# Kernel optimization log

Hardware: AMD Instinct MI355X
Metric: run time of the kernel (lower is better)

## Reference

```python
import jax, jax.numpy as jnp
import numpy as np

K = 3
KK = K * K


def conv3x3(x, w, b):
    # x: [B,C,H,W], w: [O,C,3,3]
    y = jax.lax.conv_general_dilated(x, w, (1, 1), ((1, 1), (1, 1)),
                                     dimension_numbers=('NCHW', 'OIHW', 'NCHW'))
    return y + b[None, :, None, None]


def deform_conv(x, offset, w, b):
    # torchvision.ops.deform_conv2d, 3x3, pad=1, stride=1, no mask.
    B, C, H, W = x.shape
    off = offset.reshape(B, KK, 2, H, W)  # per kernel tap: (dy, dx)
    ky = jnp.repeat(jnp.arange(K, dtype=x.dtype) - 1, K)  # [9]
    kx = jnp.tile(jnp.arange(K, dtype=x.dtype) - 1, K)
    py = jnp.arange(H, dtype=x.dtype)[None, None, :, None] + ky[None, :, None, None] + off[:, :, 0]
    px = jnp.arange(W, dtype=x.dtype)[None, None, None, :] + kx[None, :, None, None] + off[:, :, 1]
    y0 = jnp.floor(py)
    x0 = jnp.floor(px)
    wy = (py - y0)[:, None]  # [B,1,9,H,W]
    wx = (px - x0)[:, None]
    y0i = y0.astype(jnp.int32)
    x0i = x0.astype(jnp.int32)
    xf = x.reshape(B, C, H * W)

    def corner(yi, xi):
        valid = ((yi >= 0) & (yi < H) & (xi >= 0) & (xi < W))
        idx = jnp.clip(yi, 0, H - 1) * W + jnp.clip(xi, 0, W - 1)  # [B,9,H,W]
        g = jax.vmap(lambda xb, ib: xb[:, ib.reshape(-1)])(xf, idx)  # [B,C,9*H*W]
        return g.reshape(B, C, KK, H, W) * valid[:, None].astype(x.dtype)

    val = (corner(y0i, x0i) * (1 - wy) * (1 - wx)
           + corner(y0i, x0i + 1) * (1 - wy) * wx
           + corner(y0i + 1, x0i) * wy * (1 - wx)
           + corner(y0i + 1, x0i + 1) * wy * wx)  # [B,C,9,H,W]
    out = jnp.einsum('bckhw,ock->bohw', val, w.reshape(w.shape[0], C, KK))
    return out + b[None, :, None, None]


def se_gate(x, w1, b1, w2, b2):
    # global avg pool -> 1x1 conv -> relu -> 1x1 conv -> sigmoid -> scale
    m = x.mean((2, 3))  # [B,C]
    h = jax.nn.relu(jnp.einsum('bc,rc->br', m, w1) + b1)
    g = jax.nn.sigmoid(jnp.einsum('br,cr->bc', h, w2) + b2)
    return x * g[:, :, None, None]


def resize_bilinear(x, oh, ow):
    # F.interpolate(mode='bilinear', align_corners=False)
    B, C, H, W = x.shape

    def coords(n_in, n_out):
        src = (jnp.arange(n_out, dtype=x.dtype) + 0.5) * (n_in / n_out) - 0.5
        src = jnp.clip(src, 0.0, n_in - 1)
        i0 = jnp.floor(src).astype(jnp.int32)
        i1 = jnp.minimum(i0 + 1, n_in - 1)
        return i0, i1, (src - i0).astype(x.dtype)

    y0, y1, wy = coords(H, oh)
    x = x[:, :, y0, :] * (1 - wy)[None, None, :, None] + x[:, :, y1, :] * wy[None, None, :, None]
    c0, c1, wc = coords(W, ow)
    x = x[:, :, :, c0] * (1 - wc)[None, None, None, :] + x[:, :, :, c1] * wc[None, None, None, :]
    return x


def setup_inputs() -> dict:
    key = jax.random.key(0)
    ks = jax.random.split(key, 12)
    B, C, H, W = 4, 64, 128, 128
    L, O, R = 4, 64, 4  # levels, out_channels, reduction=64//16
    d = {
        'x': jax.random.normal(ks[0], (B, C, H, W), jnp.float32),
        'off_w': jax.random.normal(ks[1], (L, 2 * KK, C, 3, 3), jnp.float32) * 0.01,
        'off_b': jax.random.normal(ks[2], (L, 2 * KK), jnp.float32) * 0.01,
        'dc_w': jax.random.normal(ks[3], (L, O, C, 3, 3), jnp.float32) * 0.05,
        'dc_b': jax.random.normal(ks[4], (L, O), jnp.float32) * 0.05,
        'se_w1': jax.random.normal(ks[5], (L, R, O), jnp.float32) * 0.1,
        'se_b1': jax.random.normal(ks[6], (L, R), jnp.float32) * 0.1,
        'se_w2': jax.random.normal(ks[7], (L, O, R), jnp.float32) * 0.1,
        'se_b2': jax.random.normal(ks[8], (L, O), jnp.float32) * 0.1,
        'fuse_w': jax.random.normal(ks[9], (O, L * O), jnp.float32) * 0.05,
        'fuse_b': jax.random.normal(ks[10], (O,), jnp.float32) * 0.05,
    }
    return d


def reference(x, off_w, off_b, dc_w, dc_b, se_w1, se_b1, se_w2, se_b2, fuse_w, fuse_b):
    B, _, H, W = x.shape
    L = off_w.shape[0]
    cur = x
    feats = []
    for i in range(L):
        if i > 0:
            cur = resize_bilinear(cur, cur.shape[2] // 2, cur.shape[3] // 2)
        off = conv3x3(cur, off_w[i], off_b[i])
        cur = deform_conv(cur, off, dc_w[i], dc_b[i])
        cur = se_gate(cur, se_w1[i], se_b1[i], se_w2[i], se_b2[i])
        feats.append(resize_bilinear(cur, H, W))
    for i in range(L - 2, -1, -1):
        feats[i] = feats[i] + feats[i + 1]
    fused = jnp.concatenate(feats, axis=1)  # [B, L*O, H, W]
    return jnp.einsum('bchw,oc->bohw', fused, fuse_w) + fuse_b[None, :, None, None]
```

## Files before the change

### kernel.cpp

```cpp
#include <hip/hip_runtime.h>
#include <hip/hip_bf16.h>
#include <math.h>


constexpr int Bn = 4;

typedef __attribute__((ext_vector_type(8))) short short8;
typedef __attribute__((ext_vector_type(4))) float f32x4;
typedef __attribute__((ext_vector_type(4))) unsigned uint4v;

static __device__ __forceinline__ short f2b(float f){
  union { float f; unsigned u; } v; v.f = f;
  unsigned r = v.u + 0x7fffu + ((v.u >> 16) & 1u);
  return (short)(r >> 16);
}
static __device__ __forceinline__ unsigned f2b2(float x, float y){
  union { __hip_bfloat162 h; unsigned u; } cv;
  cv.h = __float22bfloat162_rn(make_float2(x, y));
  return cv.u;
}

constexpr size_t OFF_CUR   = 0;
constexpr size_t OFF_DC    = OFF_CUR  + 4194304;
constexpr size_t OFF_T0    = OFF_DC   + 4194304;
constexpr size_t OFF_T1    = OFF_T0   + 4194304;
constexpr size_t OFF_T2    = OFF_T1   + 1048576;
constexpr size_t OFF_T3    = OFF_T2   + 262144;
constexpr size_t OFF_WSUMT = OFF_T3   + 65536;
constexpr size_t OFF_DCWT  = OFF_WSUMT + 8192;
constexpr size_t OFF_OWT   = OFF_DCWT  + 73728;
constexpr size_t OFF_SUMS  = OFF_OWT   + 36864;

__global__ void prep_k(const float* __restrict__ dc_w, const float* __restrict__ off_w,
                       const float* __restrict__ fuse_w, float* __restrict__ ws){
  int i = blockIdx.x * 256 + threadIdx.x;
  short* dcwT  = (short*)(ws + OFF_DCWT);
  short* owT   = (short*)(ws + OFF_OWT);
  short* wsumT = (short*)(ws + OFF_WSUMT);
  if (i < 147456){
    int oc = i / 576, r = i % 576, k = r >> 6, c = r & 63;
    dcwT[i] = f2b(dc_w[(oc*64 + c)*9 + k]);
  } else if (i < 147456 + 73728){
    int t = i - 147456;
    int lm = t / 576, l = lm >> 5, m = lm & 31, r = t % 576, k = r >> 6, c = r & 63;
    owT[t] = (m < 18) ? f2b(off_w[((l*18 + m)*64 + c)*9 + k]) : (short)0;
  } else if (i < 147456 + 73728 + 16384){
    int t = i - (147456 + 73728);
    int l = t / 4096, r = t % 4096, o = r / 64, c = r % 64;
    float s = 0.f;
    for (int jl = 0; jl <= l; jl++) s += fuse_w[o*256 + jl*64 + c];
    wsumT[t] = f2b(s);
  } else if (i < 147456 + 73728 + 16384 + 65536){
    ws[OFF_SUMS + (i - (147456 + 73728 + 16384))] = 0.f;
  }
}

__global__ __launch_bounds__(256) void cvt_k(const float* __restrict__ x, float* __restrict__ cur){
  __shared__ float t[64][65];
  int tile = blockIdx.x;
  int b = tile >> 8, p0 = (tile & 255) << 6;
  int tx = threadIdx.x & 63, ty = threadIdx.x >> 6;
  #pragma unroll
  for (int c = ty; c < 64; c += 4)
    t[c][tx] = x[(((size_t)(b << 6) + c) << 14) + p0 + tx];
  __syncthreads();
  #pragma unroll
  for (int pp = ty; pp < 64; pp += 4)
    cur[(((size_t)(b << 14)) + p0 + pp) * 64 + tx] = t[tx][pp];
}

template<int H, int LVL>
__global__ __launch_bounds__(256, 6) void deform_k(
    const float* __restrict__ cur, const float* __restrict__ ws_all,
    const float* __restrict__ off_bias, const float* __restrict__ dc_bias,
    float* __restrict__ dc, float* __restrict__ sums){
  constexpr int W = H, P = H * W;
  constexpr int PITCHB = 584 * 2;
  __shared__ __align__(16) short valA[16][584];
  __shared__ float offsP[2][16][18];
  __shared__ float4 tapW[144];
  __shared__ int4   tapI[144];
  const short* owt = (const short*)(ws_all + OFF_OWT) + LVL * 32 * 576;
  const short* dcw = (const short*)(ws_all + OFF_DCWT) + (size_t)LVL * 64 * 576;
  const int tid = threadIdx.x;
  const int wave = tid >> 6, lane = tid & 63;
  const int c0 = lane & 15, quad = lane >> 4, q4 = quad * 4;
  const int half = lane >> 5, cc = lane & 31;
  const int pix0 = blockIdx.x * 16;
  const int b = pix0 / P, pb = pix0 % P;
  const int hrow = pb / W, wcol = pb % W;
  const float* curb = cur + (size_t)b * P * 64;
  const char* curc = (const char*)curb + cc * 8;
  char* valc = (char*)valA + wave * (4 * PITCHB);

  #pragma unroll
  for (int i = 0; i < 18; i++){
    const int t0 = 2*i, t1 = t0 + 1;
    const int p0 = t0/9, k0 = t0%9, p1 = t1/9, k1 = t1%9;
    int yy0 = hrow + k0/3 - 1, xx0 = wcol + wave*4 + p0 + k0%3 - 1;
    int yy1 = hrow + k1/3 - 1, xx1 = wcol + wave*4 + p1 + k1%3 - 1;
    bool v0 = ((unsigned)yy0 < (unsigned)H) & ((unsigned)xx0 < (unsigned)W);
    bool v1 = ((unsigned)yy1 < (unsigned)H) & ((unsigned)xx1 < (unsigned)W);
    int  i0 = v0 ? (yy0*W + xx0) : 0,  i1 = v1 ? (yy1*W + xx1) : 0;
    float m0 = v0 ? 1.f : 0.f,         m1 = v1 ? 1.f : 0.f;
    int   idx = half ? i1 : i0;
    float m   = half ? m1 : m0;
    float2 v = *(const float2*)(curc + (size_t)idx * 256);
    unsigned pk = f2b2(v.x * m, v.y * m);
    const int ob0 = p0*PITCHB + k0*128, ob1 = p1*PITCHB + k1*128;
    *(unsigned*)(valc + (half ? ob1 : ob0) + cc*4) = pk;
  }
  __syncthreads();

  {
    const int colw = wave & 1, kh = wave >> 1;
    f32x4 oacc = {0,0,0,0};
    #pragma unroll
    for (int kb = 0; kb < 9; kb++){
      int kk = kh*9 + kb;
      short8 a  = *(const short8*)&valA[c0][kk*32 + quad*8];
      short8 bf = *(const short8*)&owt[(colw*16 + c0)*576 + kk*32 + quad*8];
      oacc = __builtin_amdgcn_mfma_f32_16x16x32_bf16(a, bf, oacc, 0, 0, 0);
    }
    int comp = colw*16 + c0;
    if (comp < 18){
      #pragma unroll
      for (int r = 0; r < 4; r++) offsP[kh][q4 + r][comp] = oacc[r];
    }
  }
  __syncthreads();

  if (tid < 144){
    int p = tid / 9, k = tid % 9;
    int h = hrow, w = wcol + p;
    float oy = offsP[0][p][2*k]     + offsP[1][p][2*k]     + off_bias[LVL*18 + 2*k];
    float ox = offsP[0][p][2*k + 1] + offsP[1][p][2*k + 1] + off_bias[LVL*18 + 2*k + 1];
    float py = (float)(h + k/3 - 1) + oy;
    float px = (float)(w + k%3 - 1) + ox;
    float y0f = floorf(py), x0f = floorf(px);
    float fy = py - y0f, fx = px - x0f;
    int y0 = (int)y0f, x0 = (int)x0f, y1 = y0 + 1, x1 = x0 + 1;
    bool vy0 = (y0 >= 0) & (y0 < H), vy1 = (y1 >= 0) & (y1 < H);
    bool vx0 = (x0 >= 0) & (x0 < W), vx1 = (x1 >= 0) & (x1 < W);
    int y0c = min(max(y0, 0), H-1), y1c = min(max(y1, 0), H-1);
    int x0c = min(max(x0, 0), W-1), x1c = min(max(x1, 0), W-1);
    float gy = 1.f - fy, gx = 1.f - fx;
    tapW[tid] = make_float4((vy0 & vx0) ? gy*gx : 0.f,
                            (vy0 & vx1) ? gy*fx : 0.f,
                            (vy1 & vx0) ? fy*gx : 0.f,
                            (vy1 & vx1) ? fy*fx : 0.f);
    tapI[tid] = make_int4((y0c*W + x0c) << 8, (y0c*W + x1c) << 8,
                          (y1c*W + x0c) << 8, (y1c*W + x1c) << 8);
  }
  __syncthreads();

  #pragma unroll
  for (int i = 0; i < 18; i++){
    int T = wave*36 + 2*i + half;
    float4 wv = tapW[T];
    int4   ti = tapI[T];
    float2 a0 = *(const float2*)(curc + ti.x);
    float2 a1 = *(const float2*)(curc + ti.y);
    float2 a2 = *(const float2*)(curc + ti.z);
    float2 a3 = *(const float2*)(curc + ti.w);
    float vx = wv.x*a0.x + wv.y*a1.x + wv.z*a2.x + wv.w*a3.x;
    float vy = wv.x*a0.y + wv.y*a1.y + wv.z*a2.y + wv.w*a3.y;
    unsigned pk = f2b2(vx, vy);
    const int t0 = 2*i, t1 = t0 + 1;
    const int ob0 = (t0/9)*PITCHB + (t0%9)*128, ob1 = (t1/9)*PITCHB + (t1%9)*128;
    *(unsigned*)(valc + (half ? ob1 : ob0) + cc*4) = pk;
  }
  __syncthreads();

  const int n = wave*16 + c0;
  float bt = dc_bias[LVL*64 + n];
  f32x4 d0 = {bt, bt, bt, bt}, d1 = {0,0,0,0};
  #pragma unroll
  for (int kb = 0; kb < 9; kb++){
    short8 a  = *(const short8*)&valA[c0][kb*32 + quad*8];
    short8 bf = *(const short8*)&dcw[n*576 + kb*32 + quad*8];
    d0 = __builtin_amdgcn_mfma_f32_16x16x32_bf16(a, bf, d0, 0, 0, 0);
  }
  #pragma unroll
  for (int kb = 9; kb < 18; kb++){
    short8 a  = *(const short8*)&valA[c0][kb*32 + quad*8];
    short8 bf = *(const short8*)&dcw[n*576 + kb*32 + quad*8];
    d1 = __builtin_amdgcn_mfma_f32_16x16x32_bf16(a, bf, d1, 0, 0, 0);
  }
  f32x4 acc;
  #pragma unroll
  for (int r = 0; r < 4; r++) acc[r] = d0[r] + d1[r];
  float* dcb = dc + (size_t)pix0 * 64;
  #pragma unroll
  for (int r = 0; r < 4; r++) dcb[(q4 + r)*64 + n] = acc[r];
  float s = acc[0] + acc[1] + acc[2] + acc[3];
  s += __shfl_xor(s, 16);
  s += __shfl_xor(s, 32);
  if (quad == 0) atomicAdd(&sums[(LVL*16 + (blockIdx.x & 15))*256 + (b << 6) + n], s);
}

template<int W, int LVL>
__global__ __launch_bounds__(256) void fuse_gd_k(
    const float* __restrict__ dcv, const float* __restrict__ sums,
    const float* __restrict__ se_w1, const float* __restrict__ se_b1,
    const float* __restrict__ se_w2, const float* __restrict__ se_b2,
    const float* __restrict__ ws_all, float* __restrict__ tmp, float* __restrict__ curn){
  constexpr int P = W * W;
  constexpr bool POOL = (LVL < 3);
  constexpr float invP = 1.f / (float)P;
  __shared__ __align__(16) float fS[64][68];
  __shared__ __align__(16) float gsh[64];
  const short* wsl = (const short*)(ws_all + OFF_WSUMT) + LVL * 4096;
  const int tid = threadIdx.x, wave = tid >> 6, lane = tid & 63;
  const int c0 = lane & 15, quad = lane >> 4, q4 = quad * 4;
  int b, rp = 0, cs = 0;
  if (POOL){
    constexpr int tilesPerB = P / 64, tilesPerRow = W / 32;
    b = blockIdx.x / tilesPerB;
    int r = blockIdx.x % tilesPerB;
    rp = r / tilesPerRow; cs = r % tilesPerRow;
  } else {
    b = (blockIdx.x * 64) / P;
  }

  {
    int sg = tid >> 6, c = tid & 63;
    float part = 0.f;
    #pragma unroll
    for (int s = 0; s < 4; s++) part += sums[(LVL*16 + sg*4 + s)*256 + (b << 6) + c];
    fS[sg][c] = part;
    __syncthreads();
    if (tid < 64){
      int r = tid & 3, j = tid >> 2;
      float hp = 0.f;
      #pragma unroll
      for (int q = 0; q < 4; q++){
        int cq = j*4 + q;
        float m = (fS[0][cq] + fS[1][cq] + fS[2][cq] + fS[3][cq]) * invP;
        hp += m * se_w1[(LVL*4 + r)*64 + cq];
      }
      hp += __shfl_xor(hp, 4);  hp += __shfl_xor(hp, 8);
      hp += __shfl_xor(hp, 16); hp += __shfl_xor(hp, 32);
      float hr = fmaxf(hp + se_b1[LVL*4 + r], 0.f);
      float a = se_b2[LVL*64 + tid];
      #pragma unroll
      for (int r2 = 0; r2 < 4; r2++)
        a += __shfl(hr, r2) * se_w2[(LVL*64 + tid)*4 + r2];
      gsh[tid] = 1.f / (1.f + expf(-a));
    }
    __syncthreads();
  }

  float4 g4 = *(const float4*)&gsh[c0*4];
  #pragma unroll
  for (int i = 0; i < 4; i++){
    int lp = wave*16 + (lane >> 4) + i*4;
    size_t gpix = POOL ? ((size_t)b*P + (size_t)(2*rp + (lp >> 5))*W + cs*32 + (lp & 31))
                       : ((size_t)blockIdx.x*64 + lp);
    float4 d = *(const float4*)&dcv[gpix*64 + c0*4];
    float4 v = make_float4(d.x*g4.x, d.y*g4.y, d.z*g4.z, d.w*g4.w);
    *(float4*)&fS[lp][c0*4] = v;
  }
  __syncthreads();
  f32x4 acc[4] = {{0,0,0,0},{0,0,0,0},{0,0,0,0},{0,0,0,0}};
  #pragma unroll
  for (int kb = 0; kb < 2; kb++){
    float4 lo = *(const float4*)&fS[wave*16 + c0][kb*32 + quad*8];
    float4 hi = *(const float4*)&fS[wave*16 + c0][kb*32 + quad*8 + 4];
    uint4v ua = {f2b2(lo.x, lo.y), f2b2(lo.z, lo.w), f2b2(hi.x, hi.y), f2b2(hi.z, hi.w)};
    short8 a = __builtin_bit_cast(short8, ua);
    #pragma unroll
    for (int t = 0; t < 4; t++){
      short8 bf = *(const short8*)&wsl[(t*16 + c0)*64 + kb*32 + quad*8];
      acc[t] = __builtin_amdgcn_mfma_f32_16x16x32_bf16(a, bf, acc[t], 0, 0, 0);
    }
  }
  #pragma unroll
  for (int t = 0; t < 4; t++){
    int n = t*16 + c0;
    size_t plane = ((size_t)(b << 6) + n) * P;
    size_t pix = POOL ? ((size_t)(2*rp + (wave >> 1))*W + cs*32 + (wave & 1)*16 + q4)
                      : ((size_t)(blockIdx.x*64) - (size_t)b*P + wave*16 + q4);
    *(f32x4*)&tmp[plane + pix] = acc[t];
  }
  if constexpr (POOL){
    int j = tid >> 4, uu = tid & 15;
    float4 p0 = *(const float4*)&fS[2*j][uu*4];
    float4 p1 = *(const float4*)&fS[2*j + 1][uu*4];
    float4 p2 = *(const float4*)&fS[32 + 2*j][uu*4];
    float4 p3 = *(const float4*)&fS[33 + 2*j][uu*4];
    float4 av = make_float4(0.25f*(p0.x + p1.x + p2.x + p3.x),
                            0.25f*(p0.y + p1.y + p2.y + p3.y),
                            0.25f*(p0.z + p1.z + p2.z + p3.z),
                            0.25f*(p0.w + p1.w + p2.w + p3.w));
    *(float4*)&curn[((size_t)b*(P/4) + (size_t)rp*(W/2) + cs*16 + j)*64 + uu*4] = av;
  }
}

__global__ void final_k(const float* __restrict__ ws_all, const float* __restrict__ fuse_bias,
                        float* __restrict__ out){
  int i = blockIdx.x * 256 + threadIdx.x;
  int w = i & 127, h = (i >> 7) & 127, o = (i >> 14) & 63, b = i >> 20;
  float acc = fuse_bias[o] + ws_all[OFF_T0 + (((size_t)(b << 6) + o) << 14) + (h << 7) + w];
  const float* tarr[3] = {ws_all + OFF_T1, ws_all + OFF_T2, ws_all + OFF_T3};
  #pragma unroll
  for (int li = 0; li < 3; li++){
    int l = li + 1, Hl = 128 >> l;
    float scale = 1.0f / (float)(1 << l);
    float sy = fminf(fmaxf((h + 0.5f)*scale - 0.5f, 0.f), (float)(Hl - 1));
    float sx = fminf(fmaxf((w + 0.5f)*scale - 0.5f, 0.f), (float)(Hl - 1));
    int y0 = (int)sy, x0 = (int)sx;
    float fy = sy - y0, fx = sx - x0;
    int y1 = min(y0 + 1, Hl - 1), x1 = min(x0 + 1, Hl - 1);
    const float* tb = tarr[li] + (size_t)((b << 6) + o) * Hl * Hl;
    float v00 = tb[y0*Hl + x0], v01 = tb[y0*Hl + x1];
    float v10 = tb[y1*Hl + x0], v11 = tb[y1*Hl + x1];
    acc += (1.f-fy)*((1.f-fx)*v00 + fx*v01) + fy*((1.f-fx)*v10 + fx*v11);
  }
  out[i] = acc;
}

extern "C" void kernel_launch(void* const* d_in, const int* in_sizes, int n_in,
                              void* d_out, int out_size, void* d_ws, size_t ws_size,
                              hipStream_t stream){
  (void)in_sizes; (void)n_in; (void)out_size; (void)ws_size;
  const float* x      = (const float*)d_in[0];
  const float* off_w  = (const float*)d_in[1];
  const float* off_b  = (const float*)d_in[2];
  const float* dc_w   = (const float*)d_in[3];
  const float* dc_b   = (const float*)d_in[4];
  const float* se_w1  = (const float*)d_in[5];
  const float* se_b1  = (const float*)d_in[6];
  const float* se_w2  = (const float*)d_in[7];
  const float* se_b2  = (const float*)d_in[8];
  const float* fuse_w = (const float*)d_in[9];
  const float* fuse_b = (const float*)d_in[10];
  float* out = (float*)d_out;
  float* ws = (float*)d_ws;
  float* cur  = ws + OFF_CUR;
  float* dc   = ws + OFF_DC;
  float* tmp[4] = {ws + OFF_T0, ws + OFF_T1, ws + OFF_T2, ws + OFF_T3};
  float* sums = ws + OFF_SUMS;

  prep_k<<<(303104 + 255)/256, 256, 0, stream>>>(dc_w, off_w, fuse_w, ws);
  cvt_k<<<1024, 256, 0, stream>>>(x, cur);

  deform_k<128,0><<<4096, 256, 0, stream>>>(cur, ws, off_b, dc_b, dc, sums);
  fuse_gd_k<128,0><<<1024, 256, 0, stream>>>(dc, sums, se_w1, se_b1, se_w2, se_b2, ws, tmp[0], cur);
  deform_k<64,1><<<1024, 256, 0, stream>>>(cur, ws, off_b, dc_b, dc, sums);
  fuse_gd_k<64,1><<<256, 256, 0, stream>>>(dc, sums, se_w1, se_b1, se_w2, se_b2, ws, tmp[1], cur);
  deform_k<32,2><<<256, 256, 0, stream>>>(cur, ws, off_b, dc_b, dc, sums);
  fuse_gd_k<32,2><<<64, 256, 0, stream>>>(dc, sums, se_w1, se_b1, se_w2, se_b2, ws, tmp[2], cur);
  deform_k<16,3><<<64, 256, 0, stream>>>(cur, ws, off_b, dc_b, dc, sums);
  fuse_gd_k<16,3><<<16, 256, 0, stream>>>(dc, sums, se_w1, se_b1, se_w2, se_b2, ws, tmp[3], nullptr);

  final_k<<<16384, 256, 0, stream>>>(ws, fuse_b, out);
}
```

Before: 273.3 us.

## Store intermediate activations as bf16 and tile deform blocks as 4x4 pixel squares

The NHWC activation buffer feeding the deformable conv is now packed as bf16 pairs instead of fp32, in both the initial transpose and the pooled output of the fuse kernel. This halves gather bytes for the 3x3 taps and the bilinear corner samples. Each block also now covers a 4x4 spatial tile instead of 16 pixels in one row, which should improve cache locality of the neighbour gathers. The cost is an extra rounding of the input to bf16 before the bilinear interpolation, which slightly changes numerics.

```diff
diff --git a/kernel.cpp b/kernel.cpp
--- a/kernel.cpp
+++ b/kernel.cpp
@@ -19,6 +19,8 @@
   cv.h = __float22bfloat162_rn(make_float2(x, y));
   return cv.u;
 }
+static __device__ __forceinline__ float blo(unsigned u){ return __uint_as_float(u << 16); }
+static __device__ __forceinline__ float bhi(unsigned u){ return __uint_as_float(u & 0xffff0000u); }
 
 constexpr size_t OFF_CUR   = 0;
 constexpr size_t OFF_DC    = OFF_CUR  + 4194304;
@@ -55,7 +57,7 @@
   }
 }
 
-__global__ __launch_bounds__(256) void cvt_k(const float* __restrict__ x, float* __restrict__ cur){
+__global__ __launch_bounds__(256) void cvt_k(const float* __restrict__ x, unsigned* __restrict__ cur){
   __shared__ float t[64][65];
   int tile = blockIdx.x;
   int b = tile >> 8, p0 = (tile & 255) << 6;
@@ -64,18 +66,23 @@
   for (int c = ty; c < 64; c += 4)
     t[c][tx] = x[(((size_t)(b << 6) + c) << 14) + p0 + tx];
   __syncthreads();
-  #pragma unroll
-  for (int pp = ty; pp < 64; pp += 4)
-    cur[(((size_t)(b << 14)) + p0 + pp) * 64 + tx] = t[tx][pp];
+  int u = threadIdx.x & 31, pr = threadIdx.x >> 5;
+  #pragma unroll
+  for (int i = 0; i < 8; i++){
+    int pp = pr + i*8;
+    unsigned v = f2b2(t[2*u][pp], t[2*u + 1][pp]);
+    cur[((size_t)(b << 14) + p0 + pp)*32 + u] = v;
+  }
 }
 
 template<int H, int LVL>
 __global__ __launch_bounds__(256, 6) void deform_k(
-    const float* __restrict__ cur, const float* __restrict__ ws_all,
+    const unsigned* __restrict__ cur, const float* __restrict__ ws_all,
     const float* __restrict__ off_bias, const float* __restrict__ dc_bias,
     float* __restrict__ dc, float* __restrict__ sums){
   constexpr int W = H, P = H * W;
   constexpr int PITCHB = 584 * 2;
+  constexpr int TPR = W/4, TPB = P/16;
   __shared__ __align__(16) short valA[16][584];
   __shared__ float offsP[2][16][18];
   __shared__ float4 tapW[144];
@@ -86,29 +93,27 @@
   const int wave = tid >> 6, lane = tid & 63;
   const int c0 = lane & 15, quad = lane >> 4, q4 = quad * 4;
   const int half = lane >> 5, cc = lane & 31;
-  const int pix0 = blockIdx.x * 16;
-  const int b = pix0 / P, pb = pix0 % P;
-  const int hrow = pb / W, wcol = pb % W;
-  const float* curb = cur + (size_t)b * P * 64;
-  const char* curc = (const char*)curb + cc * 8;
+  const int b = blockIdx.x / TPB;
+  const int rr = blockIdx.x % TPB;
+  const int hrow = (rr / TPR) * 4, wcol = (rr % TPR) * 4;
+  const char* curc = (const char*)(cur + (size_t)b * P * 32) + cc * 4;
   char* valc = (char*)valA + wave * (4 * PITCHB);
 
   #pragma unroll
   for (int i = 0; i < 18; i++){
     const int t0 = 2*i, t1 = t0 + 1;
-    const int p0 = t0/9, k0 = t0%9, p1 = t1/9, k1 = t1%9;
-    int yy0 = hrow + k0/3 - 1, xx0 = wcol + wave*4 + p0 + k0%3 - 1;
-    int yy1 = hrow + k1/3 - 1, xx1 = wcol + wave*4 + p1 + k1%3 - 1;
+    const int p0l = t0/9, k0 = t0%9, p1l = t1/9, k1 = t1%9;
+    int yy0 = hrow + wave + k0/3 - 1, xx0 = wcol + p0l + k0%3 - 1;
+    int yy1 = hrow + wave + k1/3 - 1, xx1 = wcol + p1l + k1%3 - 1;
     bool v0 = ((unsigned)yy0 < (unsigned)H) & ((unsigned)xx0 < (unsigned)W);
     bool v1 = ((unsigned)yy1 < (unsigned)H) & ((unsigned)xx1 < (unsigned)W);
     int  i0 = v0 ? (yy0*W + xx0) : 0,  i1 = v1 ? (yy1*W + xx1) : 0;
-    float m0 = v0 ? 1.f : 0.f,         m1 = v1 ? 1.f : 0.f;
     int   idx = half ? i1 : i0;
-    float m   = half ? m1 : m0;
-    float2 v = *(const float2*)(curc + (size_t)idx * 256);
-    unsigned pk = f2b2(v.x * m, v.y * m);
-    const int ob0 = p0*PITCHB + k0*128, ob1 = p1*PITCHB + k1*128;
-    *(unsigned*)(valc + (half ? ob1 : ob0) + cc*4) = pk;
+    bool  vv  = half ? v1 : v0;
+    unsigned uv = *(const unsigned*)(curc + (size_t)idx * 128);
+    uv = vv ? uv : 0u;
+    const int ob0 = p0l*PITCHB + k0*128, ob1 = p1l*PITCHB + k1*128;
+    *(unsigned*)(valc + (half ? ob1 : ob0) + cc*4) = uv;
   }
   __syncthreads();
 
@@ -132,7 +137,7 @@
 
   if (tid < 144){
     int p = tid / 9, k = tid % 9;
-    int h = hrow, w = wcol + p;
+    int h = hrow + (p >> 2), w = wcol + (p & 3);
     float oy = offsP[0][p][2*k]     + offsP[1][p][2*k]     + off_bias[LVL*18 + 2*k];
     float ox = offsP[0][p][2*k + 1] + offsP[1][p][2*k + 1] + off_bias[LVL*18 + 2*k + 1];
     float py = (float)(h + k/3 - 1) + oy;
@@ -149,8 +154,8 @@
                             (vy0 & vx1) ? gy*fx : 0.f,
                             (vy1 & vx0) ? fy*gx : 0.f,
                             (vy1 & vx1) ? fy*fx : 0.f);
-    tapI[tid] = make_int4((y0c*W + x0c) << 8, (y0c*W + x1c) << 8,
-                          (y1c*W + x0c) << 8, (y1c*W + x1c) << 8);
+    tapI[tid] = make_int4((y0c*W + x0c) << 7, (y0c*W + x1c) << 7,
+                          (y1c*W + x0c) << 7, (y1c*W + x1c) << 7);
   }
   __syncthreads();
 
@@ -159,12 +164,12 @@
     int T = wave*36 + 2*i + half;
     float4 wv = tapW[T];
     int4   ti = tapI[T];
-    float2 a0 = *(const float2*)(curc + ti.x);
-    float2 a1 = *(const float2*)(curc + ti.y);
-    float2 a2 = *(const float2*)(curc + ti.z);
-    float2 a3 = *(const float2*)(curc + ti.w);
-    float vx = wv.x*a0.x + wv.y*a1.x + wv.z*a2.x + wv.w*a3.x;
-    float vy = wv.x*a0.y + wv.y*a1.y + wv.z*a2.y + wv.w*a3.y;
+    unsigned u0 = *(const unsigned*)(curc + ti.x);
+    unsigned u1 = *(const unsigned*)(curc + ti.y);
+    unsigned u2 = *(const unsigned*)(curc + ti.z);
+    unsigned u3 = *(const unsigned*)(curc + ti.w);
+    float vx = wv.x*blo(u0) + wv.y*blo(u1) + wv.z*blo(u2) + wv.w*blo(u3);
+    float vy = wv.x*bhi(u0) + wv.y*bhi(u1) + wv.z*bhi(u2) + wv.w*bhi(u3);
     unsigned pk = f2b2(vx, vy);
     const int t0 = 2*i, t1 = t0 + 1;
     const int ob0 = (t0/9)*PITCHB + (t0%9)*128, ob1 = (t1/9)*PITCHB + (t1%9)*128;
@@ -173,8 +178,8 @@
   __syncthreads();
 
   const int n = wave*16 + c0;
-  float bt = dc_bias[LVL*64 + n];
-  f32x4 d0 = {bt, bt, bt, bt}, d1 = {0,0,0,0};
+  float bt2 = dc_bias[LVL*64 + n];
+  f32x4 d0 = {bt2, bt2, bt2, bt2}, d1 = {0,0,0,0};
   #pragma unroll
   for (int kb = 0; kb < 9; kb++){
     short8 a  = *(const short8*)&valA[c0][kb*32 + quad*8];
@@ -190,9 +195,9 @@
   f32x4 acc;
   #pragma unroll
   for (int r = 0; r < 4; r++) acc[r] = d0[r] + d1[r];
-  float* dcb = dc + (size_t)pix0 * 64;
-  #pragma unroll
-  for (int r = 0; r < 4; r++) dcb[(q4 + r)*64 + n] = acc[r];
+  float* dcb = dc + ((size_t)b*P + (size_t)(hrow + quad)*W + wcol)*64;
+  #pragma unroll
+  for (int r = 0; r < 4; r++) dcb[r*64 + n] = acc[r];
   float s = acc[0] + acc[1] + acc[2] + acc[3];
   s += __shfl_xor(s, 16);
   s += __shfl_xor(s, 32);
@@ -204,7 +209,7 @@
     const float* __restrict__ dcv, const float* __restrict__ sums,
     const float* __restrict__ se_w1, const float* __restrict__ se_b1,
     const float* __restrict__ se_w2, const float* __restrict__ se_b2,
-    const float* __restrict__ ws_all, float* __restrict__ tmp, float* __restrict__ curn){
+    const float* __restrict__ ws_all, float* __restrict__ tmp, unsigned* __restrict__ curn){
   constexpr int P = W * W;
   constexpr bool POOL = (LVL < 3);
   constexpr float invP = 1.f / (float)P;
@@ -293,7 +298,8 @@
                             0.25f*(p0.y + p1.y + p2.y + p3.y),
                             0.25f*(p0.z + p1.z + p2.z + p3.z),
                             0.25f*(p0.w + p1.w + p2.w + p3.w));
-    *(float4*)&curn[((size_t)b*(P/4) + (size_t)rp*(W/2) + cs*16 + j)*64 + uu*4] = av;
+    uint2 pv = make_uint2(f2b2(av.x, av.y), f2b2(av.z, av.w));
+    *(uint2*)&curn[((size_t)b*(P/4) + (size_t)rp*(W/2) + cs*16 + j)*32 + uu*2] = pv;
   }
 }
 
@@ -337,7 +343,7 @@
   const float* fuse_b = (const float*)d_in[10];
   float* out = (float*)d_out;
   float* ws = (float*)d_ws;
-  float* cur  = ws + OFF_CUR;
+  unsigned* cur = (unsigned*)(ws + OFF_CUR);
   float* dc   = ws + OFF_DC;
   float* tmp[4] = {ws + OFF_T0, ws + OFF_T1, ws + OFF_T2, ws + OFF_T3};
   float* sums = ws + OFF_SUMS;
```

New measurement: 234.4 us. 14.2% less time.
